# Kernel optimization log

Measured on AMD Instinct MI355X. Metric: run time of the kernel, lower is better.

Reference implementation:

```python
import jax, jax.numpy as jnp
import numpy as np

N = 131072
D = 512        # input_dim
H = 512        # hidden_dim
E = 10         # num_experts
INIT_STD_SCALE = 0.1


def _trunc_normal(key, shape, std):
    # approximate trunc_normal_(std=std) in [-2std, 2std]
    return jnp.clip(jax.random.normal(key, shape) * std, -2.0 * std, 2.0 * std).astype(jnp.float32)


def setup_inputs() -> dict:
    key = jax.random.key(0)
    ks = jax.random.split(key, 6)
    x = jax.random.normal(ks[0], (N, D), dtype=jnp.float32)
    # router (default nn.Linear init approximated with uniform)
    lim = 1.0 / np.sqrt(D)
    Wr = jax.random.uniform(ks[1], (E, D), minval=-lim, maxval=lim, dtype=jnp.float32)
    br = jnp.zeros((E,), dtype=jnp.float32)
    # experts: trunc_normal with std = 0.1 / sqrt(fan_in), zero bias
    W1 = _trunc_normal(ks[2], (E, D, H), INIT_STD_SCALE / np.sqrt(D))   # [E, D, H]
    b1 = jnp.zeros((E, H), dtype=jnp.float32)
    W2 = _trunc_normal(ks[3], (E, H, H), INIT_STD_SCALE / np.sqrt(H))   # [E, H, H]
    b2 = jnp.zeros((E, H), dtype=jnp.float32)
    return {"x": x, "Wr": Wr, "br": br, "W1": W1, "b1": b1, "W2": W2, "b2": b2}


def reference(x, Wr, br, W1, b1, W2, b2):
    # router in fp32 (autocast disabled in original)
    logits = x.astype(jnp.float32) @ Wr.T + br          # [N, E]
    expert_ids = jnp.argmax(logits, axis=1)              # [N]
    out = jnp.zeros((x.shape[0], W2.shape[-1]), dtype=x.dtype)
    # fixed small loop over experts; dropout is identity at inference
    for e in range(W1.shape[0]):
        h = jax.nn.relu(x @ W1[e] + b1[e])                # [N, H]
        o = h @ W2[e] + b2[e]                             # [N, H]
        out = jnp.where((expert_ids == e)[:, None], o, out)
    return out, expert_ids
```

## Files before the change

### kernel.cpp

```cpp
#include <hip/hip_runtime.h>
#include <hip/hip_bf16.h>

#define N_TOK 131072
#define DIM   512
#define HID   512
#define NEXP  10

using bf16x8 = __attribute__((ext_vector_type(8))) short;
using f32x4  = __attribute__((ext_vector_type(4))) float;

__device__ __forceinline__ short f2bf(float f) {
    union { float f; unsigned u; } v; v.f = f;
    unsigned u = v.u;
    return (short)((u + 0x7FFFu + ((u >> 16) & 1u)) >> 16);
}

#define GLOAD16(g, l) __builtin_amdgcn_global_load_lds( \
    (const __attribute__((address_space(1))) void*)(g),  \
    (__attribute__((address_space(3))) void*)(l), 16, 0, 0)

__global__ __launch_bounds__(256) void router_kernel(
    const float* __restrict__ x, const float* __restrict__ Wr,
    const float* __restrict__ br, int* __restrict__ eid,
    float* __restrict__ ids_out, int* __restrict__ counts,
    short* __restrict__ xb)
{
    __shared__ float wr[NEXP][DIM];
    __shared__ int lcnt[NEXP];
    int tid = threadIdx.x;
    for (int i = tid; i < NEXP * DIM / 4; i += 256)
        ((float4*)wr)[i] = ((const float4*)Wr)[i];
    if (tid < NEXP) lcnt[tid] = 0;
    __syncthreads();

    int lane  = tid & 63;
    int wave  = tid >> 6;
    int gwave = blockIdx.x * 4 + wave;
    int nwav  = gridDim.x * 4;

    for (int t = gwave; t < N_TOK; t += nwav) {
        const float4* xr = (const float4*)(x + (size_t)t * DIM);
        float4 v0 = xr[lane * 2], v1 = xr[lane * 2 + 1];
        float xf[8] = {v0.x, v0.y, v0.z, v0.w, v1.x, v1.y, v1.z, v1.w};
        bf16x8 p;
        #pragma unroll
        for (int j = 0; j < 8; ++j) p[j] = f2bf(xf[j]);
        *(bf16x8*)(xb + (size_t)t * DIM + lane * 8) = p;

        float dot[NEXP];
        #pragma unroll
        for (int e = 0; e < NEXP; ++e) {
            const float* wv = &wr[e][lane * 8];
            float s = 0.f;
            #pragma unroll
            for (int j = 0; j < 8; ++j) s = fmaf(xf[j], wv[j], s);
            dot[e] = s;
        }
        #pragma unroll
        for (int off = 32; off > 0; off >>= 1) {
            #pragma unroll
            for (int e = 0; e < NEXP; ++e) dot[e] += __shfl_xor(dot[e], off, 64);
        }
        if (lane == 0) {
            int best = 0; float bv = dot[0] + br[0];
            #pragma unroll
            for (int e = 1; e < NEXP; ++e) {
                float v = dot[e] + br[e];
                if (v > bv) { bv = v; best = e; }
            }
            eid[t] = best;
            ids_out[t] = (float)best;
            atomicAdd(&lcnt[best], 1);
        }
    }
    __syncthreads();
    if (tid < NEXP) atomicAdd(&counts[tid], lcnt[tid]);
}

__global__ void offsets_kernel(const int* __restrict__ counts,
                               int* __restrict__ offsets, int* __restrict__ toff)
{
    if (threadIdx.x == 0) {
        int acc = 0, ta = 0;
        for (int e = 0; e < NEXP; ++e) {
            offsets[e] = acc; toff[e] = ta;
            acc += counts[e]; ta += (counts[e] + 255) >> 8;
        }
        offsets[NEXP] = acc; toff[NEXP] = ta;
    }
}

__global__ __launch_bounds__(256) void scatter_kernel(
    const int* __restrict__ eid, const int* __restrict__ offsets,
    int* __restrict__ cursors, int* __restrict__ perm)
{
    __shared__ int lcnt[NEXP], lbase[NEXP];
    int tid = threadIdx.x;
    if (tid < NEXP) lcnt[tid] = 0;
    __syncthreads();
    int t = blockIdx.x * 256 + tid;
    int e = 0, lpos = 0;
    if (t < N_TOK) {
        e = eid[t];
        lpos = atomicAdd(&lcnt[e], 1);
    }
    __syncthreads();
    if (tid < NEXP) lbase[tid] = atomicAdd(&cursors[tid], lcnt[tid]);
    __syncthreads();
    if (t < N_TOK) perm[offsets[e] + lbase[e] + lpos] = t;
}

__global__ __launch_bounds__(256) void wconvert_kernel(
    const float* __restrict__ W1, const float* __restrict__ W2,
    short* __restrict__ W1b, short* __restrict__ W2b)
{
    int mat = blockIdx.z;
    const float* src = (mat < NEXP) ? W1 + (size_t)mat * 512 * 512
                                    : W2 + (size_t)(mat - NEXP) * 512 * 512;
    short* dst = (mat < NEXP) ? W1b + (size_t)mat * 512 * 512
                              : W2b + (size_t)(mat - NEXP) * 512 * 512;
    __shared__ float tile[64][65];
    int r0 = blockIdx.y * 64, c0 = blockIdx.x * 64;
    int tid = threadIdx.x;
    int tr = tid >> 4, tc4 = (tid & 15) * 4;
    #pragma unroll
    for (int i = 0; i < 4; ++i) {
        float4 v = *(const float4*)(src + (size_t)(r0 + i * 16 + tr) * 512 + c0 + tc4);
        tile[i * 16 + tr][tc4 + 0] = v.x; tile[i * 16 + tr][tc4 + 1] = v.y;
        tile[i * 16 + tr][tc4 + 2] = v.z; tile[i * 16 + tr][tc4 + 3] = v.w;
    }
    __syncthreads();
    int s   = (r0 + tc4) >> 5;
    int kin = (r0 + tc4) & 31;
    #pragma unroll
    for (int i = 0; i < 4; ++i) {
        int cc = i * 16 + tr;
        ushort4 o;
        o.x = (ushort)f2bf(tile[tc4 + 0][cc]); o.y = (ushort)f2bf(tile[tc4 + 1][cc]);
        o.z = (ushort)f2bf(tile[tc4 + 2][cc]); o.w = (ushort)f2bf(tile[tc4 + 3][cc]);
        *(ushort4*)(dst + (size_t)s * 16384 + (size_t)(c0 + cc) * 32 + kin) = o;
    }
}

template<int LAYER>
__global__ __launch_bounds__(1024, 2) void expert_gemm(
    const short* __restrict__ xb, const short* __restrict__ hA,
    const short* __restrict__ WT, const float* __restrict__ bias,
    const int* __restrict__ offsets, const int* __restrict__ toff,
    const int* __restrict__ perm,
    short* __restrict__ hOut, float* __restrict__ out)
{
    int g = blockIdx.x;
    if (g >= toff[NEXP]) return;
    int e = 0;
    #pragma unroll
    for (int k = 1; k < NEXP; ++k) e += (g >= toff[k]);
    int beg = offsets[e], cnt = offsets[e + 1] - beg;
    int m0 = (g - toff[e]) * 256;
    int nb = blockIdx.y * 256;

    __shared__ int toks[256];
    __shared__ short Ab[2][256 * 32];
    __shared__ short Bb[2][256 * 32];

    int tid = threadIdx.x, lane = tid & 63, w = tid >> 6;
    if (tid < 256) toks[tid] = perm[beg + min(m0 + tid, cnt - 1)];
    __syncthreads();

    const short* WTe = WT + (size_t)e * 512 * 512;
    int srow = tid >> 2;
    int kqp  = tid & 3;
    int ql   = kqp ^ ((srow >> 1) & 3);
    const short* aS;
    if (LAYER == 1) aS = xb + (size_t)toks[srow] * DIM + ql * 8;
    else            aS = hA + (size_t)(beg + min(m0 + srow, cnt - 1)) * HID + ql * 8;
    const short* bS = WTe + (size_t)(nb + srow) * 32 + ql * 8;

    auto stage = [&](int t, int b) {
        GLOAD16(bS + t * 16384, (char*)&Bb[b][0] + tid * 16);
        GLOAD16(aS + t * 32,    (char*)&Ab[b][0] + tid * 16);
    };

    int wr = w >> 2, wc = w & 3, lrow = lane & 15, kq = lane >> 4;
    int offA[4], offB[4];
    #pragma unroll
    for (int i = 0; i < 4; ++i) {
        int r = wr * 64 + i * 16 + lrow;
        offA[i] = r * 64 + (kq ^ ((r >> 1) & 3)) * 16;
    }
    #pragma unroll
    for (int j = 0; j < 4; ++j) {
        int r = wc * 64 + j * 16 + lrow;
        offB[j] = r * 64 + (kq ^ ((r >> 1) & 3)) * 16;
    }

    f32x4 acc[4][4];
    #pragma unroll
    for (int i = 0; i < 4; ++i)
        #pragma unroll
        for (int j = 0; j < 4; ++j) acc[i][j] = (f32x4){0.f, 0.f, 0.f, 0.f};

    auto comp = [&](int b) {
        bf16x8 af[4], bv[4];
        #pragma unroll
        for (int i = 0; i < 4; ++i) af[i] = *(const bf16x8*)((char*)&Ab[b][0] + offA[i]);
        #pragma unroll
        for (int j = 0; j < 4; ++j) bv[j] = *(const bf16x8*)((char*)&Bb[b][0] + offB[j]);
        __builtin_amdgcn_s_setprio(1);
        #pragma unroll
        for (int i = 0; i < 4; ++i)
            #pragma unroll
            for (int j = 0; j < 4; ++j)
                acc[i][j] = __builtin_amdgcn_mfma_f32_16x16x32_bf16(af[i], bv[j], acc[i][j], 0, 0, 0);
        __builtin_amdgcn_s_setprio(0);
    };

    stage(0, 0);
    stage(1, 1);
    asm volatile("s_waitcnt vmcnt(2)" ::: "memory");
    __builtin_amdgcn_s_barrier();

    #pragma unroll
    for (int t = 0; t < 16; ++t) {
        comp(t & 1);
        if (t == 15) break;
        __builtin_amdgcn_s_barrier();
        asm volatile("" ::: "memory");
        if (t + 2 < 16) {
            stage(t + 2, t & 1);
            asm volatile("s_waitcnt vmcnt(2)" ::: "memory");
        } else {
            asm volatile("s_waitcnt vmcnt(0)" ::: "memory");
        }
        __builtin_amdgcn_s_barrier();
    }

    const float* be = bias + (size_t)e * 512;
    int colb = nb + wc * 64 + lrow;
    float bvv[4];
    #pragma unroll
    for (int j = 0; j < 4; ++j) bvv[j] = be[colb + j * 16];

    #pragma unroll
    for (int i = 0; i < 4; ++i) {
        #pragma unroll
        for (int q = 0; q < 4; ++q) {
            int rr = wr * 64 + i * 16 + kq * 4 + q;
            if (m0 + rr < cnt) {
                if (LAYER == 1) {
                    short* hp = hOut + (size_t)(beg + m0 + rr) * HID + colb;
                    #pragma unroll
                    for (int j = 0; j < 4; ++j) {
                        float v = acc[i][j][q] + bvv[j];
                        hp[j * 16] = f2bf(v > 0.f ? v : 0.f);
                    }
                } else {
                    float* op = out + (size_t)toks[rr] * HID + colb;
                    #pragma unroll
                    for (int j = 0; j < 4; ++j)
                        op[j * 16] = acc[i][j][q] + bvv[j];
                }
            }
        }
    }
}

extern "C" void kernel_launch(void* const* d_in, const int* in_sizes, int n_in,
                              void* d_out, int out_size, void* d_ws, size_t ws_size,
                              hipStream_t stream)
{
    const float* x  = (const float*)d_in[0];
    const float* Wr = (const float*)d_in[1];
    const float* br = (const float*)d_in[2];
    const float* W1 = (const float*)d_in[3];
    const float* b1 = (const float*)d_in[4];
    const float* W2 = (const float*)d_in[5];
    const float* b2 = (const float*)d_in[6];

    float* out     = (float*)d_out;
    float* ids_out = out + (size_t)N_TOK * HID;

    char* ws     = (char*)d_ws;
    int* counts  = (int*)ws;
    int* offsets = counts + 16;
    int* toff    = counts + 32;
    int* cursors = counts + 48;
    int* eid     = (int*)(ws + 1024);
    int* perm    = eid + N_TOK;
    short* W1b   = (short*)(ws + 1024 + (size_t)2 * N_TOK * 4);
    short* W2b   = W1b + (size_t)NEXP * 512 * 512;
    short* h     = W2b + (size_t)NEXP * 512 * 512;
    short* xb    = h   + (size_t)N_TOK * HID;

    hipMemsetAsync(d_ws, 0, 1024, stream);
    router_kernel<<<2048, 256, 0, stream>>>(x, Wr, br, eid, ids_out, counts, xb);
    wconvert_kernel<<<dim3(8, 8, 2 * NEXP), 256, 0, stream>>>(W1, W2, W1b, W2b);
    offsets_kernel<<<1, 64, 0, stream>>>(counts, offsets, toff);
    scatter_kernel<<<512, 256, 0, stream>>>(eid, offsets, cursors, perm);

    int ntiles = (N_TOK + 255) / 256 + NEXP;
    expert_gemm<1><<<dim3(ntiles, 2), 1024, 0, stream>>>(xb, nullptr, W1b, b1, offsets, toff, perm, h, nullptr);
    expert_gemm<2><<<dim3(ntiles, 2), 1024, 0, stream>>>(nullptr, h, W2b, b2, offsets, toff, perm, nullptr, out);
}
```

Measured before the change: 364.7 us.

## Use 512-thread blocks with 128x64 per-wave tiles and half-step pipelined staging

Halves the expert GEMM block to 8 waves, so each wave now accumulates a 128x64 output tile (8x4 MFMA fragments) instead of 64x64. That raises register-level reuse of the B fragments. The K loop now advances 64 per iteration, split into four quarter-phases, and the next tile's A/B halves are issued between them to overlap global-to-LDS loads with MFMA work. The shared buffer grows to about 129KB, which likely limits occupancy to one block per CU. Accumulator register pressure also doubles per thread.

```diff
diff --git a/kernel.cpp b/kernel.cpp
--- a/kernel.cpp
+++ b/kernel.cpp
@@ -143,7 +143,7 @@
 }
 
 template<int LAYER>
-__global__ __launch_bounds__(1024, 2) void expert_gemm(
+__global__ __launch_bounds__(512, 2) void expert_gemm(
     const short* __restrict__ xb, const short* __restrict__ hA,
     const short* __restrict__ WT, const float* __restrict__ bias,
     const int* __restrict__ offsets, const int* __restrict__ toff,
@@ -159,9 +159,8 @@
     int m0 = (g - toff[e]) * 256;
     int nb = blockIdx.y * 256;
 
-    __shared__ int toks[256];
-    __shared__ short Ab[2][256 * 32];
-    __shared__ short Bb[2][256 * 32];
+    __shared__ char SMEM[132096];
+    int* toks = (int*)(SMEM + 131072);
 
     int tid = threadIdx.x, lane = tid & 63, w = tid >> 6;
     if (tid < 256) toks[tid] = perm[beg + min(m0 + tid, cnt - 1)];
@@ -171,68 +170,89 @@
     int srow = tid >> 2;
     int kqp  = tid & 3;
     int ql   = kqp ^ ((srow >> 1) & 3);
-    const short* aS;
-    if (LAYER == 1) aS = xb + (size_t)toks[srow] * DIM + ql * 8;
-    else            aS = hA + (size_t)(beg + min(m0 + srow, cnt - 1)) * HID + ql * 8;
+    const short *aS0, *aS1;
+    if (LAYER == 1) {
+        aS0 = xb + (size_t)toks[srow] * DIM + ql * 8;
+        aS1 = xb + (size_t)toks[srow + 128] * DIM + ql * 8;
+    } else {
+        aS0 = hA + (size_t)(beg + min(m0 + srow, cnt - 1)) * HID + ql * 8;
+        aS1 = hA + (size_t)(beg + min(m0 + srow + 128, cnt - 1)) * HID + ql * 8;
+    }
     const short* bS = WTe + (size_t)(nb + srow) * 32 + ql * 8;
 
-    auto stage = [&](int t, int b) {
-        GLOAD16(bS + t * 16384, (char*)&Bb[b][0] + tid * 16);
-        GLOAD16(aS + t * 32,    (char*)&Ab[b][0] + tid * 16);
+    int wr = w >> 2, wc = w & 3, lrow = lane & 15, kq = lane >> 4;
+    int offA[8], offB[4];
+    #pragma unroll
+    for (int f = 0; f < 8; ++f) {
+        int r = wr * 128 + f * 16 + lrow;
+        offA[f] = r * 64 + ((kq ^ ((r >> 1) & 3)) << 4);
+    }
+    #pragma unroll
+    for (int j = 0; j < 4; ++j) {
+        int c = wc * 64 + j * 16 + lrow;
+        offB[j] = c * 64 + ((kq ^ ((c >> 1) & 3)) << 4);
+    }
+
+    f32x4 acc[8][4];
+    #pragma unroll
+    for (int f = 0; f < 8; ++f)
+        #pragma unroll
+        for (int j = 0; j < 4; ++j) acc[f][j] = (f32x4){0.f, 0.f, 0.f, 0.f};
+
+    auto stage_half = [&](int t, int p, int b) {
+        int kh = p >> 1;
+        if ((p & 1) == 0) {
+            GLOAD16(aS0 + t * 64 + kh * 32, SMEM + b * 32768 + kh * 16384 + tid * 16);
+            GLOAD16(aS1 + t * 64 + kh * 32, SMEM + b * 32768 + kh * 16384 + 8192 + tid * 16);
+        } else {
+            const short* s = bS + (size_t)(t * 2 + kh) * 16384;
+            GLOAD16(s,        SMEM + 65536 + b * 32768 + kh * 16384 + tid * 16);
+            GLOAD16(s + 4096, SMEM + 65536 + b * 32768 + kh * 16384 + 8192 + tid * 16);
+        }
     };
 
-    int wr = w >> 2, wc = w & 3, lrow = lane & 15, kq = lane >> 4;
-    int offA[4], offB[4];
-    #pragma unroll
-    for (int i = 0; i < 4; ++i) {
-        int r = wr * 64 + i * 16 + lrow;
-        offA[i] = r * 64 + (kq ^ ((r >> 1) & 3)) * 16;
-    }
-    #pragma unroll
-    for (int j = 0; j < 4; ++j) {
-        int r = wc * 64 + j * 16 + lrow;
-        offB[j] = r * 64 + (kq ^ ((r >> 1) & 3)) * 16;
-    }
-
-    f32x4 acc[4][4];
-    #pragma unroll
-    for (int i = 0; i < 4; ++i)
-        #pragma unroll
-        for (int j = 0; j < 4; ++j) acc[i][j] = (f32x4){0.f, 0.f, 0.f, 0.f};
-
-    auto comp = [&](int b) {
-        bf16x8 af[4], bv[4];
-        #pragma unroll
-        for (int i = 0; i < 4; ++i) af[i] = *(const bf16x8*)((char*)&Ab[b][0] + offA[i]);
-        #pragma unroll
-        for (int j = 0; j < 4; ++j) bv[j] = *(const bf16x8*)((char*)&Bb[b][0] + offB[j]);
-        __builtin_amdgcn_s_setprio(1);
-        #pragma unroll
-        for (int i = 0; i < 4; ++i)
-            #pragma unroll
-            for (int j = 0; j < 4; ++j)
-                acc[i][j] = __builtin_amdgcn_mfma_f32_16x16x32_bf16(af[i], bv[j], acc[i][j], 0, 0, 0);
-        __builtin_amdgcn_s_setprio(0);
-    };
-
-    stage(0, 0);
-    stage(1, 1);
-    asm volatile("s_waitcnt vmcnt(2)" ::: "memory");
+    stage_half(0, 0, 0); stage_half(0, 1, 0); stage_half(0, 2, 0); stage_half(0, 3, 0);
+    asm volatile("s_waitcnt vmcnt(4)" ::: "memory");
     __builtin_amdgcn_s_barrier();
 
-    #pragma unroll
-    for (int t = 0; t < 16; ++t) {
-        comp(t & 1);
-        if (t == 15) break;
-        __builtin_amdgcn_s_barrier();
-        asm volatile("" ::: "memory");
-        if (t + 2 < 16) {
-            stage(t + 2, t & 1);
-            asm volatile("s_waitcnt vmcnt(2)" ::: "memory");
-        } else {
-            asm volatile("s_waitcnt vmcnt(0)" ::: "memory");
-        }
-        __builtin_amdgcn_s_barrier();
+    bf16x8 bv[4];
+    #pragma unroll
+    for (int t = 0; t < 8; ++t) {
+        int b = t & 1;
+        #pragma unroll
+        for (int p = 0; p < 4; ++p) {
+            int kh = p >> 1, rh = p & 1;
+            const char* ABp = SMEM + b * 32768 + kh * 16384;
+            const char* BBp = SMEM + 65536 + b * 32768 + kh * 16384;
+            bf16x8 af[4];
+            if (rh == 0) {
+                #pragma unroll
+                for (int j = 0; j < 4; ++j) bv[j] = *(const bf16x8*)(BBp + offB[j]);
+            }
+            #pragma unroll
+            for (int i = 0; i < 4; ++i) af[i] = *(const bf16x8*)(ABp + offA[rh * 4 + i]);
+
+            if (t < 7) stage_half(t + 1, p, b ^ 1);
+
+            if (p == 1) {
+                if (t < 7) asm volatile("s_waitcnt vmcnt(4)" ::: "memory");
+                else       asm volatile("s_waitcnt vmcnt(0)" ::: "memory");
+            } else if (p == 3 && t < 7) {
+                asm volatile("s_waitcnt vmcnt(4)" ::: "memory");
+            }
+            __builtin_amdgcn_s_barrier();
+            asm volatile("s_waitcnt lgkmcnt(0)" ::: "memory");
+            __builtin_amdgcn_sched_barrier(0);
+            __builtin_amdgcn_s_setprio(1);
+            #pragma unroll
+            for (int i = 0; i < 4; ++i)
+                #pragma unroll
+                for (int j = 0; j < 4; ++j)
+                    acc[rh * 4 + i][j] = __builtin_amdgcn_mfma_f32_16x16x32_bf16(
+                        af[i], bv[j], acc[rh * 4 + i][j], 0, 0, 0);
+            __builtin_amdgcn_s_setprio(0);
+            if (!(t == 7 && p == 3)) __builtin_amdgcn_s_barrier();
+        }
     }
 
     const float* be = bias + (size_t)e * 512;
@@ -242,23 +262,23 @@
     for (int j = 0; j < 4; ++j) bvv[j] = be[colb + j * 16];
 
     #pragma unroll
-    for (int i = 0; i < 4; ++i) {
+    for (int f = 0; f < 8; ++f) {
         #pragma unroll
         for (int q = 0; q < 4; ++q) {
-            int rr = wr * 64 + i * 16 + kq * 4 + q;
+            int rr = wr * 128 + f * 16 + kq * 4 + q;
             if (m0 + rr < cnt) {
                 if (LAYER == 1) {
                     short* hp = hOut + (size_t)(beg + m0 + rr) * HID + colb;
                     #pragma unroll
                     for (int j = 0; j < 4; ++j) {
-                        float v = acc[i][j][q] + bvv[j];
+                        float v = acc[f][j][q] + bvv[j];
                         hp[j * 16] = f2bf(v > 0.f ? v : 0.f);
                     }
                 } else {
                     float* op = out + (size_t)toks[rr] * HID + colb;
                     #pragma unroll
                     for (int j = 0; j < 4; ++j)
-                        op[j * 16] = acc[i][j][q] + bvv[j];
+                        op[j * 16] = acc[f][j][q] + bvv[j];
                 }
             }
         }
@@ -299,6 +319,6 @@
     scatter_kernel<<<512, 256, 0, stream>>>(eid, offsets, cursors, perm);
 
     int ntiles = (N_TOK + 255) / 256 + NEXP;
-    expert_gemm<1><<<dim3(ntiles, 2), 1024, 0, stream>>>(xb, nullptr, W1b, b1, offsets, toff, perm, h, nullptr);
-    expert_gemm<2><<<dim3(ntiles, 2), 1024, 0, stream>>>(nullptr, h, W2b, b2, offsets, toff, perm, nullptr, out);
-}
+    expert_gemm<1><<<dim3(ntiles, 2), 512, 0, stream>>>(xb, nullptr, W1b, b1, offsets, toff, perm, h, nullptr);
+    expert_gemm<2><<<dim3(ntiles, 2), 512, 0, stream>>>(nullptr, h, W2b, b2, offsets, toff, perm, nullptr, out);
+}
```

Measured after the change: 365.5 us. About the same (+0.2%).
